# Performance work log

Hardware: AMD Instinct MI355X
Metric: run time of the kernel (lower is better)

## Reference

```python
import jax, jax.numpy as jnp
import numpy as np

B, C, H, W = 4, 512, 64, 64
INTER = 64  # C // channel_stride


def setup_inputs() -> dict:
    key = jax.random.key(0)
    ks = jax.random.split(key, 5)
    s = 0.02  # small init scale for numerical stability of softmax logits
    return {
        "inputs": jax.random.normal(ks[0], (B, C, H, W), dtype=jnp.float32),
        "Wq": jax.random.normal(ks[1], (INTER, C), dtype=jnp.float32) * s,
        "bq": jnp.zeros((INTER,), dtype=jnp.float32),
        "Wk": jax.random.normal(ks[2], (INTER, C), dtype=jnp.float32) * s,
        "bk": jnp.zeros((INTER,), dtype=jnp.float32),
        "Wv": jax.random.normal(ks[3], (C, C), dtype=jnp.float32) * s,
        "bv": jnp.zeros((C,), dtype=jnp.float32),
        "gamma": jax.random.normal(ks[4], (1,), dtype=jnp.float32),
    }


def reference(inputs, Wq, bq, Wk, bk, Wv, bv, gamma):
    b, c, h, w = inputs.shape
    n = h * w
    x = inputs.reshape(b, c, n)  # (B, C, N)
    # 1x1 convs == per-pixel linear projections
    q = jnp.einsum('dc,bcn->bnd', Wq, x) + bq            # (B, N, d)
    k = jnp.einsum('dc,bcn->bdn', Wk, x) + bk[:, None]   # (B, d, N)
    v = jnp.einsum('oc,bcn->bon', Wv, x) + bv[:, None]   # (B, O, N)
    # affinity: (B, Nq, Nk), softmax over keys (last dim), no scaling (as in source)
    affinity = jax.nn.softmax(jnp.einsum('bnd,bdm->bnm', q, k), axis=-1)
    # note: torch does bmm(value, affinity) -> out[b,o,m] = sum_j v[b,o,j] * A[b,j,m]
    out = jnp.einsum('bon,bnm->bom', v, affinity)        # (B, O, N)
    return gamma * out.reshape(b, -1, h, w) + inputs
```

## Files before the change

### kernel.cpp

```cpp
#include <hip/hip_runtime.h>
#include <stdint.h>

typedef __attribute__((ext_vector_type(8))) short short8;
typedef __attribute__((ext_vector_type(4))) float f32x4;
typedef __attribute__((ext_vector_type(8))) unsigned short u16x8;
typedef __attribute__((ext_vector_type(4))) unsigned short u16x4;
typedef __attribute__((ext_vector_type(2))) unsigned short u16x2;
typedef unsigned short u16;

#define NPIX 4096
#define CCH  512
#define DD   64


__device__ inline float b2f(u16 h){
  union { unsigned int i; float f; } u; u.i = ((unsigned int)h) << 16; return u.f;
}
__device__ inline u16 f2b(float f){
  union { float f; unsigned int i; } u; u.f = f;
  return (u16)((u.i + 0x7fffu + ((u.i >> 16) & 1u)) >> 16);
}
__device__ inline void gl2lds16(const void* g, void* l){
  __builtin_amdgcn_global_load_lds((const __attribute__((address_space(1))) unsigned int*)g,
                                   (__attribute__((address_space(3))) unsigned int*)l, 16, 0, 0);
}
__device__ inline f32x4 mfma16(short8 a, short8 b, f32x4 c){
  return __builtin_amdgcn_mfma_f32_16x16x32_bf16(a, b, c, 0, 0, 0);
}

__global__ __launch_bounds__(256) void k0_transpose(const float* __restrict__ x,
    u16* __restrict__ xT, const float* __restrict__ Wq, const float* __restrict__ Wk,
    const float* __restrict__ Wv, u16* __restrict__ Wqkb, u16* __restrict__ Wvb){
  if (blockIdx.z == 4){
    int bid = blockIdx.x * 8 + blockIdx.y;
    for (int r = 0; r < 3; ++r){
      int i = (r * 512 + bid) * 256 + threadIdx.x;
      if (i < 65536){
        int row = i >> 9, col = i & 511;
        float v = (row < 64) ? Wq[(row << 9) + col] : Wk[((row - 64) << 9) + col];
        Wqkb[(row << 9) + (col ^ ((row & 7) << 3))] = f2b(v);
      } else if (i < 327680){
        int j = i - 65536;
        int row = j >> 9, col = j & 511;
        Wvb[(row << 9) + (col ^ ((row & 7) << 3))] = f2b(Wv[j]);
      }
    }
    return;
  }
  __shared__ u16 tile[64][66];
  const int b = blockIdx.z;
  const int n0 = blockIdx.x * 64, c0 = blockIdx.y * 64;
  const float* xb = x + ((size_t)b * CCH + c0) * NPIX + n0;
  #pragma unroll
  for (int r = 0; r < 16; ++r){
    int id = r * 256 + threadIdx.x;
    int cc = id >> 6, nn = id & 63;
    tile[nn][cc] = f2b(xb[(size_t)cc * NPIX + nn]);
  }
  __syncthreads();
  u16* xTb = xT + ((size_t)b * NPIX + n0) * CCH + c0;
  #pragma unroll
  for (int r = 0; r < 8; ++r){
    int id = r * 256 + threadIdx.x;
    int nn = id >> 5, c2 = id & 31;
    int colp = (2 * c2) ^ ((nn & 7) << 3);
    *(u16x2*)(xTb + (size_t)nn * CCH + colp) = *(const u16x2*)&tile[nn][2 * c2];
  }
}

__global__ __launch_bounds__(256) void k1_qk(const u16* __restrict__ xT,
    const u16* __restrict__ Wqk, const float* __restrict__ bq,
    const float* __restrict__ bk, u16* __restrict__ Qb, u16* __restrict__ Kb){
  __shared__ __align__(16) u16 As[128*64];
  __shared__ __align__(16) u16 Bs[128*64];
  const int b  = blockIdx.z;
  const int n0 = blockIdx.x * 128;
  const u16* Ab = xT + ((size_t)b * NPIX + n0) * CCH;
  const int t = threadIdx.x, wave = t >> 6, lane = t & 63, q = lane >> 4, l16 = lane & 15;
  const int wr = (wave >> 1) * 64, wc = (wave & 1) * 64;
  const int sw = l16 & 7;
  f32x4 acc[4][4];
  #pragma unroll
  for (int i = 0; i < 4; ++i)
    #pragma unroll
    for (int j = 0; j < 4; ++j) acc[i][j] = (f32x4){0.f,0.f,0.f,0.f};

  for (int k0 = 0; k0 < CCH; k0 += 64){
    __syncthreads();
    #pragma unroll
    for (int r = 0; r < 4; ++r){
      int id = r * 256 + t;
      int row = id >> 3, ko = (id & 7) << 3;
      gl2lds16(Ab + (size_t)row * CCH + k0 + ko, &As[id * 8]);
      gl2lds16(Wqk + (size_t)row * CCH + k0 + ko, &Bs[id * 8]);
    }
    __syncthreads();
    #pragma unroll
    for (int s = 0; s < 2; ++s){
      const int ca = ((s*4 + q) ^ sw) << 3;
      short8 af[4], bfr[4];
      #pragma unroll
      for (int i = 0; i < 4; ++i){
        af[i]  = *(const short8*)&As[(wr + i*16 + l16)*64 + ca];
        bfr[i] = *(const short8*)&Bs[(wc + i*16 + l16)*64 + ca];
      }
      #pragma unroll
      for (int i = 0; i < 4; ++i)
        #pragma unroll
        for (int j = 0; j < 4; ++j)
          acc[i][j] = mfma16(af[i], bfr[j], acc[i][j]);
    }
  }
  #pragma unroll
  for (int i = 0; i < 4; ++i){
    #pragma unroll
    for (int j = 0; j < 4; ++j){
      int col = wc + j*16 + l16;
      #pragma unroll
      for (int r2 = 0; r2 < 4; ++r2){
        int n = n0 + wr + i*16 + q*4 + r2;
        int sw8 = (n & 7) << 3;
        float v = acc[i][j][r2];
        if (col < 64) Qb[((size_t)b * NPIX + n) * DD + (col ^ sw8)]        = f2b(v + bq[col]);
        else          Kb[((size_t)b * NPIX + n) * DD + ((col - 64) ^ sw8)] = f2b(v + bk[col - 64]);
      }
    }
  }
}

__global__ __launch_bounds__(256) void k2_v(const u16* __restrict__ xT,
    const u16* __restrict__ Wvb, const float* __restrict__ bv, u16* __restrict__ Vb){
  __shared__ __align__(16) u16 As[128*64];
  __shared__ __align__(16) u16 Bs[128*64];
  const int b  = blockIdx.z;
  const int n0 = blockIdx.x * 128;
  const int o0 = blockIdx.y * 128;
  const u16* Ab = Wvb + (size_t)o0 * CCH;
  const u16* Bb = xT + ((size_t)b * NPIX + n0) * CCH;
  const int t = threadIdx.x, wave = t >> 6, lane = t & 63, q = lane >> 4, l16 = lane & 15;
  const int wr = (wave >> 1) * 64, wc = (wave & 1) * 64;
  const int sw = l16 & 7;
  f32x4 acc[4][4];
  #pragma unroll
  for (int i = 0; i < 4; ++i)
    #pragma unroll
    for (int j = 0; j < 4; ++j) acc[i][j] = (f32x4){0.f,0.f,0.f,0.f};

  for (int k0 = 0; k0 < CCH; k0 += 64){
    __syncthreads();
    #pragma unroll
    for (int r = 0; r < 4; ++r){
      int id = r * 256 + t;
      int row = id >> 3, ko = (id & 7) << 3;
      gl2lds16(Ab + (size_t)row * CCH + k0 + ko, &As[id * 8]);
      gl2lds16(Bb + (size_t)row * CCH + k0 + ko, &Bs[id * 8]);
    }
    __syncthreads();
    #pragma unroll
    for (int s = 0; s < 2; ++s){
      const int ca = ((s*4 + q) ^ sw) << 3;
      short8 af[4], bfr[4];
      #pragma unroll
      for (int i = 0; i < 4; ++i){
        af[i]  = *(const short8*)&As[(wr + i*16 + l16)*64 + ca];
        bfr[i] = *(const short8*)&Bs[(wc + i*16 + l16)*64 + ca];
      }
      #pragma unroll
      for (int i = 0; i < 4; ++i)
        #pragma unroll
        for (int j = 0; j < 4; ++j)
          acc[i][j] = mfma16(af[i], bfr[j], acc[i][j]);
    }
  }
  #pragma unroll
  for (int i = 0; i < 4; ++i){
    #pragma unroll
    for (int j = 0; j < 4; ++j){
      int n = n0 + wc + j*16 + l16;
      #pragma unroll
      for (int r2 = 0; r2 < 4; ++r2){
        int o = o0 + wr + i*16 + q*4 + r2;
        int np = n ^ ((o & 7) << 3);
        Vb[((size_t)b * CCH + o) * NPIX + np] = f2b(acc[i][j][r2] + bv[o]);
      }
    }
  }
}

__global__ __launch_bounds__(256) void k3_logits(const u16* __restrict__ Qb,
    const u16* __restrict__ Kb, u16* __restrict__ E, float* __restrict__ Z, int b0){
  __shared__ __align__(16) u16 smem[128*136];
  u16* As = smem;
  u16* Bs = smem + 128*64;
  const int bloc = blockIdx.z, b = b0 + bloc;
  const int n0 = blockIdx.x * 128;
  const int m0 = blockIdx.y * 128;
  const u16* Ab = Kb + ((size_t)b * NPIX + m0) * DD;
  const u16* Bb = Qb + ((size_t)b * NPIX + n0) * DD;
  const int t = threadIdx.x, wave = t >> 6, lane = t & 63, q = lane >> 4, l16 = lane & 15;
  const int wr = (wave >> 1) * 64, wc = (wave & 1) * 64;
  const int sw = l16 & 7;
  f32x4 acc[4][4];
  #pragma unroll
  for (int i = 0; i < 4; ++i)
    #pragma unroll
    for (int j = 0; j < 4; ++j) acc[i][j] = (f32x4){0.f,0.f,0.f,0.f};

  #pragma unroll
  for (int r = 0; r < 4; ++r){
    int id = r * 256 + t;
    int row = id >> 3, ko = (id & 7) << 3;
    gl2lds16(Ab + row * DD + ko, &As[id * 8]);
    gl2lds16(Bb + row * DD + ko, &Bs[id * 8]);
  }
  __syncthreads();
  #pragma unroll
  for (int s = 0; s < 2; ++s){
    const int ca = ((s*4 + q) ^ sw) << 3;
    short8 af[4], bfr[4];
    #pragma unroll
    for (int i = 0; i < 4; ++i){
      af[i]  = *(const short8*)&As[(wr + i*16 + l16)*64 + ca];
      bfr[i] = *(const short8*)&Bs[(wc + i*16 + l16)*64 + ca];
    }
    #pragma unroll
    for (int i = 0; i < 4; ++i)
      #pragma unroll
      for (int j = 0; j < 4; ++j)
        acc[i][j] = mfma16(af[i], bfr[j], acc[i][j]);
  }
  __syncthreads();
  u16* tile = smem;
  float colsum[4] = {0.f, 0.f, 0.f, 0.f};
  #pragma unroll
  for (int i = 0; i < 4; ++i){
    #pragma unroll
    for (int j = 0; j < 4; ++j){
      #pragma unroll
      for (int r2 = 0; r2 < 4; ++r2){
        int mrow = wr + i*16 + q*4 + r2;
        int ncol = wc + j*16 + l16;
        float l = fminf(fmaxf(acc[i][j][r2], -60.f), 30.f);
        float e = __expf(l);
        tile[mrow * 136 + ncol] = f2b(e);
        colsum[j] += e;
      }
    }
  }
  #pragma unroll
  for (int j = 0; j < 4; ++j){
    float v = colsum[j];
    v += __shfl_xor(v, 16, 64);
    v += __shfl_xor(v, 32, 64);
    if (q == 0) atomicAdd(&Z[(size_t)b * NPIX + n0 + wc + j*16 + l16], v);
  }
  __syncthreads();
  u16* Eb = E + (size_t)bloc * NPIX * NPIX;
  #pragma unroll
  for (int r = 0; r < 8; ++r){
    int id = r * 256 + t;
    int row = id >> 4, chunk = id & 15;
    int g = chunk >> 3, c3 = chunk & 7;
    int colp = g * 64 + ((c3 ^ (row & 7)) << 3);
    *(u16x8*)(Eb + (size_t)(m0 + row) * NPIX + n0 + colp) =
        *(const u16x8*)&tile[row * 136 + chunk * 8];
  }
}

__global__ __launch_bounds__(256) void k3b_scale(u16* __restrict__ Vb,
    const float* __restrict__ Z, const float* __restrict__ gm, int b0){
  size_t i4  = ((size_t)blockIdx.x * 256 + threadIdx.x) * 4;
  size_t off = ((size_t)b0 << 21) + i4;
  int b = (int)(off >> 21);
  int o = (int)((off >> 12) & 511);
  int np = (int)(off & (NPIX - 1));
  int nl = np ^ ((o & 7) << 3);
  float g = gm[0];
  u16x4 vv = *(const u16x4*)(Vb + off);
  f32x4 zz = *(const f32x4*)(Z + ((size_t)b << 12) + nl);
  u16x4 r;
  #pragma unroll
  for (int k = 0; k < 4; ++k) r[k] = f2b(g * b2f(vv[k]) / fmaxf(zz[k], 1e-20f));
  *(u16x4*)(Vb + off) = r;
}

__global__ __launch_bounds__(512, 2) void k4_out(const u16* __restrict__ Vs,
    const u16* __restrict__ E, const float* __restrict__ xin,
    float* __restrict__ outp, int b0){
  __shared__ __align__(16) u16 smem[67584];
  u16* As = smem;
  const int bloc = blockIdx.z, b = b0 + bloc;
  const int m0 = blockIdx.x * 256;
  const int o0 = blockIdx.y * 128;
  const u16* Ab = Vs + ((size_t)b * CCH + o0) * NPIX;
  const u16* Bb = E + (size_t)bloc * NPIX * NPIX + (size_t)m0 * NPIX;
  const int t = threadIdx.x, wave = t >> 6, lane = t & 63, q = lane >> 4, l16 = lane & 15;
  const int grp = wave >> 2;
  const int br  = (wave & 3) * 64;
  const int sw = l16 & 7;
  const int ca = ((grp * 4 + q) ^ sw) << 3;
  const u16* bp = Bb + (size_t)(br + l16) * NPIX + (size_t)ca;

  auto stageA = [&](int kt, int bi){
    const int k0 = kt << 6;
    u16* dst = As + bi * (128*64);
    #pragma unroll
    for (int r = 0; r < 2; ++r){
      int id = r * 512 + t;
      gl2lds16(Ab + (size_t)(id >> 3) * NPIX + (k0 + ((id & 7) << 3)), dst + id * 8);
    }
  };

  f32x4 acc[8][4];
  #pragma unroll
  for (int i = 0; i < 8; ++i)
    #pragma unroll
    for (int j = 0; j < 4; ++j) acc[i][j] = (f32x4){0.f,0.f,0.f,0.f};

  short8 bfr[4];
  stageA(0, 0);
  #pragma unroll
  for (int j = 0; j < 4; ++j)
    bfr[j] = *(const short8*)(bp + (size_t)j * 16 * NPIX);
  asm volatile("s_waitcnt vmcnt(0)" ::: "memory");
  __builtin_amdgcn_sched_barrier(0);
  __builtin_amdgcn_s_barrier();

  for (int kt = 0; kt < NPIX / 64; ++kt){
    const int bi = kt & 1;
    const bool pf = (kt + 1) < NPIX / 64;
    const u16* Ap = As + bi * (128*64);
    short8 af[8];
    #pragma unroll
    for (int i = 0; i < 8; ++i) af[i] = *(const short8*)&Ap[(i*16 + l16)*64 + ca];
    if (pf) stageA(kt + 1, bi ^ 1);
    asm volatile("s_waitcnt lgkmcnt(0)" ::: "memory");
    __builtin_amdgcn_sched_barrier(0);
    __builtin_amdgcn_s_setprio(1);
    #pragma unroll
    for (int i = 0; i < 8; ++i)
      #pragma unroll
      for (int j = 0; j < 4; ++j)
        acc[i][j] = mfma16(af[i], bfr[j], acc[i][j]);
    __builtin_amdgcn_s_setprio(0);
    __builtin_amdgcn_sched_barrier(0);
    if (pf){
      #pragma unroll
      for (int j = 0; j < 4; ++j)
        bfr[j] = *(const short8*)(bp + (size_t)j * 16 * NPIX + ((kt + 1) << 6));
      asm volatile("s_waitcnt vmcnt(4)" ::: "memory");
    } else {
      asm volatile("s_waitcnt vmcnt(0)" ::: "memory");
    }
    __builtin_amdgcn_sched_barrier(0);
    __builtin_amdgcn_s_barrier();
  }

  float* red = (float*)smem;
  if (grp == 1){
    #pragma unroll
    for (int i = 0; i < 8; ++i)
      #pragma unroll
      for (int j = 0; j < 4; ++j)
        *(f32x4*)&red[(size_t)(br + j*16 + l16) * 132 + i*16 + q*4] = acc[i][j];
  }
  __syncthreads();
  if (grp == 0){
    const float* xb = xin + (size_t)b * CCH * NPIX;
    float* ob = outp + (size_t)b * CCH * NPIX;
    #pragma unroll
    for (int i = 0; i < 8; ++i){
      #pragma unroll
      for (int j = 0; j < 4; ++j){
        f32x4 p = *(const f32x4*)&red[(size_t)(br + j*16 + l16) * 132 + i*16 + q*4];
        int m = m0 + br + j*16 + l16;
        #pragma unroll
        for (int r2 = 0; r2 < 4; ++r2){
          int o = o0 + i*16 + q*4 + r2;
          size_t idx = (size_t)o * NPIX + m;
          ob[idx] = acc[i][j][r2] + p[r2] + xb[idx];
        }
      }
    }
  }
}

extern "C" void kernel_launch(void* const* d_in, const int* in_sizes, int n_in,
                              void* d_out, int out_size, void* d_ws, size_t ws_size,
                              hipStream_t stream){
  (void)in_sizes; (void)n_in; (void)out_size;
  const float* x  = (const float*)d_in[0];
  const float* Wq = (const float*)d_in[1];
  const float* bq = (const float*)d_in[2];
  const float* Wk = (const float*)d_in[3];
  const float* bk = (const float*)d_in[4];
  const float* Wv = (const float*)d_in[5];
  const float* bv = (const float*)d_in[6];
  const float* gm = (const float*)d_in[7];
  float* outp = (float*)d_out;

  char* ws = (char*)d_ws;
  u16*  Qb   = (u16*)(ws + 0);
  u16*  Kb   = (u16*)(ws + 2097152);
  u16*  Vb   = (u16*)(ws + 4194304);
  float* Z   = (float*)(ws + 20971520);
  u16*  Wqkb = (u16*)(ws + 21037056);
  u16*  Wvb  = (u16*)(ws + 21168128);
  u16*  xT   = (u16*)(ws + 21692416);
  u16*  E    = (u16*)(ws + 21692416);

  const size_t ebytes = (size_t)NPIX * NPIX * 2;
  const size_t base   = 21692416;
  if (ws_size < base + ebytes){
    return;
  }
  int NB = 1;
  if (ws_size >= base + 4 * ebytes) NB = 4;
  else if (ws_size >= base + 2 * ebytes) NB = 2;

  hipMemsetAsync(Z, 0, (size_t)4 * NPIX * sizeof(float), stream);
  k0_transpose<<<dim3(64, 8, 5), 256, 0, stream>>>(x, xT, Wq, Wk, Wv, Wqkb, Wvb);
  k1_qk<<<dim3(32, 1, 4), 256, 0, stream>>>(xT, Wqkb, bq, bk, Qb, Kb);
  k2_v<<<dim3(32, 4, 4), 256, 0, stream>>>(xT, Wvb, bv, Vb);
  for (int b0 = 0; b0 < 4; b0 += NB){
    int nb = NB; if (b0 + nb > 4) nb = 4 - b0;
    k3_logits<<<dim3(32, 32, nb), 256, 0, stream>>>(Qb, Kb, E, Z, b0);
    k3b_scale<<<dim3(nb * 2048), 256, 0, stream>>>(Vb, Z, gm, b0);
    k4_out<<<dim3(16, 4, nb), 512, 0, stream>>>(Vb, E, x, outp, b0);
  }
}
```

Measured before the change: 244.0 us.

## Halve k4_out block to 256 threads with double-buffered B fragments

The output GEMM kernel shrinks from 512 to 256 threads per block, covering 128 output pixels instead of 256, and launches twice as many blocks. LDS use per block is halved. The K loop is unrolled by two, with explicit A/B LDS slots and ping-pong register buffers for the E fragments, so the next tile's global loads are issued before the current MFMAs. The aim is higher occupancy and better latency hiding, at the cost of less reuse of V tiles per block and a full vmcnt(0) wait every half-step.

```diff
diff --git a/kernel.cpp b/kernel.cpp
--- a/kernel.cpp
+++ b/kernel.cpp
@@ -284,29 +284,29 @@
   *(u16x4*)(Vb + off) = r;
 }
 
-__global__ __launch_bounds__(512, 2) void k4_out(const u16* __restrict__ Vs,
+__global__ __launch_bounds__(256, 2) void k4_out(const u16* __restrict__ Vs,
     const u16* __restrict__ E, const float* __restrict__ xin,
     float* __restrict__ outp, int b0){
-  __shared__ __align__(16) u16 smem[67584];
+  __shared__ __align__(16) u16 smem[33792];
   u16* As = smem;
   const int bloc = blockIdx.z, b = b0 + bloc;
-  const int m0 = blockIdx.x * 256;
+  const int m0 = blockIdx.x * 128;
   const int o0 = blockIdx.y * 128;
   const u16* Ab = Vs + ((size_t)b * CCH + o0) * NPIX;
   const u16* Bb = E + (size_t)bloc * NPIX * NPIX + (size_t)m0 * NPIX;
   const int t = threadIdx.x, wave = t >> 6, lane = t & 63, q = lane >> 4, l16 = lane & 15;
-  const int grp = wave >> 2;
-  const int br  = (wave & 3) * 64;
+  const int grp = wave >> 1;
+  const int br  = (wave & 1) * 64;
   const int sw = l16 & 7;
   const int ca = ((grp * 4 + q) ^ sw) << 3;
   const u16* bp = Bb + (size_t)(br + l16) * NPIX + (size_t)ca;
 
-  auto stageA = [&](int kt, int bi){
+  auto stageA = [&](int kt, int slot){
     const int k0 = kt << 6;
-    u16* dst = As + bi * (128*64);
-    #pragma unroll
-    for (int r = 0; r < 2; ++r){
-      int id = r * 512 + t;
+    u16* dst = As + slot * (128*64);
+    #pragma unroll
+    for (int r = 0; r < 4; ++r){
+      int id = r * 256 + t;
       gl2lds16(Ab + (size_t)(id >> 3) * NPIX + (k0 + ((id & 7) << 3)), dst + id * 8);
     }
   };
@@ -317,43 +317,62 @@
     #pragma unroll
     for (int j = 0; j < 4; ++j) acc[i][j] = (f32x4){0.f,0.f,0.f,0.f};
 
-  short8 bfr[4];
+  short8 bfrA[4], bfrB[4];
   stageA(0, 0);
   #pragma unroll
   for (int j = 0; j < 4; ++j)
-    bfr[j] = *(const short8*)(bp + (size_t)j * 16 * NPIX);
+    bfrA[j] = *(const short8*)(bp + (size_t)j * 16 * NPIX);
   asm volatile("s_waitcnt vmcnt(0)" ::: "memory");
   __builtin_amdgcn_sched_barrier(0);
   __builtin_amdgcn_s_barrier();
 
-  for (int kt = 0; kt < NPIX / 64; ++kt){
-    const int bi = kt & 1;
-    const bool pf = (kt + 1) < NPIX / 64;
-    const u16* Ap = As + bi * (128*64);
-    short8 af[8];
-    #pragma unroll
-    for (int i = 0; i < 8; ++i) af[i] = *(const short8*)&Ap[(i*16 + l16)*64 + ca];
-    if (pf) stageA(kt + 1, bi ^ 1);
-    asm volatile("s_waitcnt lgkmcnt(0)" ::: "memory");
-    __builtin_amdgcn_sched_barrier(0);
-    __builtin_amdgcn_s_setprio(1);
-    #pragma unroll
-    for (int i = 0; i < 8; ++i)
+  for (int kt = 0; kt < NPIX / 64; kt += 2){
+    {
+      short8 af[8];
+      #pragma unroll
+      for (int i = 0; i < 8; ++i) af[i] = *(const short8*)&As[(i*16 + l16)*64 + ca];
       #pragma unroll
       for (int j = 0; j < 4; ++j)
-        acc[i][j] = mfma16(af[i], bfr[j], acc[i][j]);
-    __builtin_amdgcn_s_setprio(0);
-    __builtin_amdgcn_sched_barrier(0);
-    if (pf){
-      #pragma unroll
-      for (int j = 0; j < 4; ++j)
-        bfr[j] = *(const short8*)(bp + (size_t)j * 16 * NPIX + ((kt + 1) << 6));
-      asm volatile("s_waitcnt vmcnt(4)" ::: "memory");
-    } else {
+        bfrB[j] = *(const short8*)(bp + (size_t)j * 16 * NPIX + (size_t)((kt + 1) << 6));
+      stageA(kt + 1, 1);
+      asm volatile("s_waitcnt lgkmcnt(0)" ::: "memory");
+      __builtin_amdgcn_sched_barrier(0);
+      __builtin_amdgcn_s_setprio(1);
+      #pragma unroll
+      for (int i = 0; i < 8; ++i)
+        #pragma unroll
+        for (int j = 0; j < 4; ++j)
+          acc[i][j] = mfma16(af[i], bfrA[j], acc[i][j]);
+      __builtin_amdgcn_s_setprio(0);
       asm volatile("s_waitcnt vmcnt(0)" ::: "memory");
-    }
-    __builtin_amdgcn_sched_barrier(0);
-    __builtin_amdgcn_s_barrier();
+      __builtin_amdgcn_sched_barrier(0);
+      __builtin_amdgcn_s_barrier();
+    }
+    {
+      const bool pf = (kt + 2) < NPIX / 64;
+      short8 af[8];
+      #pragma unroll
+      for (int i = 0; i < 8; ++i)
+        af[i] = *(const short8*)&As[128*64 + (i*16 + l16)*64 + ca];
+      if (pf){
+        #pragma unroll
+        for (int j = 0; j < 4; ++j)
+          bfrA[j] = *(const short8*)(bp + (size_t)j * 16 * NPIX + (size_t)((kt + 2) << 6));
+        stageA(kt + 2, 0);
+      }
+      asm volatile("s_waitcnt lgkmcnt(0)" ::: "memory");
+      __builtin_amdgcn_sched_barrier(0);
+      __builtin_amdgcn_s_setprio(1);
+      #pragma unroll
+      for (int i = 0; i < 8; ++i)
+        #pragma unroll
+        for (int j = 0; j < 4; ++j)
+          acc[i][j] = mfma16(af[i], bfrB[j], acc[i][j]);
+      __builtin_amdgcn_s_setprio(0);
+      asm volatile("s_waitcnt vmcnt(0)" ::: "memory");
+      __builtin_amdgcn_sched_barrier(0);
+      __builtin_amdgcn_s_barrier();
+    }
   }
 
   float* red = (float*)smem;
@@ -426,6 +445,6 @@
     int nb = NB; if (b0 + nb > 4) nb = 4 - b0;
     k3_logits<<<dim3(32, 32, nb), 256, 0, stream>>>(Qb, Kb, E, Z, b0);
     k3b_scale<<<dim3(nb * 2048), 256, 0, stream>>>(Vb, Z, gm, b0);
-    k4_out<<<dim3(16, 4, nb), 512, 0, stream>>>(Vb, E, x, outp, b0);
-  }
-}
+    k4_out<<<dim3(32, 4, nb), 256, 0, stream>>>(Vb, E, x, outp, b0);
+  }
+}
```

Result: faster. 237.4 us (-2.7%).
